# Performance work log

Measured on AMD Instinct MI355X. Metric: run time of the kernel, lower is better.

## Reference

```python
import jax, jax.numpy as jnp
import numpy as np

EMBED_DIM = 768
NUM_HEADS = 12
PROJ_DIM = EMBED_DIM // NUM_HEADS  # 64
M_FEATURES = 128
EPS = 1e-6


def _orthogonal_projection(key, m, d):
    # Faithful to create_projection_matrix(scaling=0): stacked transposed Q-factors
    # of iid gaussian blocks, rescaled by chi-distributed row norms.
    nb_full_blocks = m // d
    keys = jax.random.split(key, nb_full_blocks + 2)
    blocks = []
    for i in range(nb_full_blocks):
        q, _ = jnp.linalg.qr(jax.random.normal(keys[i], (d, d)))
        blocks.append(q.T)
    rem = m - nb_full_blocks * d
    if rem > 0:
        q, _ = jnp.linalg.qr(jax.random.normal(keys[nb_full_blocks], (d, d)))
        blocks.append(q.T[:rem])
    final = jnp.vstack(blocks)
    multiplier = jnp.linalg.norm(jax.random.normal(keys[-1], (m, d)), axis=1)
    return multiplier[:, None] * final


def setup_inputs() -> dict:
    key = jax.random.key(0)
    ks = jax.random.split(key, 8)
    B, L, E = 4, 4096, EMBED_DIM
    s = 1.0 / np.sqrt(E)
    inp = {
        "x": jax.random.normal(ks[0], (B, L, E), jnp.float32),
        "Wq": jax.random.normal(ks[1], (E, E), jnp.float32) * s,
        "bq": jnp.zeros((E,), jnp.float32),
        "Wk": jax.random.normal(ks[2], (E, E), jnp.float32) * s,
        "bk": jnp.zeros((E,), jnp.float32),
        "Wv": jax.random.normal(ks[3], (E, E), jnp.float32) * s,
        "bv": jnp.zeros((E,), jnp.float32),
        "Wo": jax.random.normal(ks[4], (E, E), jnp.float32) * s,
        "bo": jnp.zeros((E,), jnp.float32),
        "proj": _orthogonal_projection(ks[5], M_FEATURES, PROJ_DIM),
    }
    return inp


def _softmax_kernel(data, projection_matrix):
    # data: [B, L, H, D]; projection_matrix: [M, D]
    data_normalizer = 1.0 / jnp.sqrt(jnp.sqrt(jnp.float32(PROJ_DIM)))
    data = data_normalizer * data
    ratio = 1.0 / jnp.sqrt(jnp.float32(projection_matrix.shape[0]))
    data_dash = jnp.einsum("blhd,md->blhm", data, projection_matrix)
    diag_data = jnp.sum(jnp.square(data), axis=-1, keepdims=True) / 2.0  # [B,L,H,1]
    stab = jnp.max(data_dash, axis=-1, keepdims=True)
    return ratio * (jnp.exp(data_dash - diag_data - stab) + EPS)


def reference(x, Wq, bq, Wk, bk, Wv, bv, Wo, bo, proj):
    B, L, E = x.shape
    H, D = NUM_HEADS, PROJ_DIM

    def split_heads(t):
        return t.reshape(B, L, H, D)

    q = split_heads(x @ Wq + bq)
    k = split_heads(x @ Wk + bk)
    v = split_heads(x @ Wv + bv)

    q_prime = _softmax_kernel(q, proj)  # [B,L,H,M]
    k_prime = _softmax_kernel(k, proj)  # [B,L,H,M]

    # Linear-attention numerator/denominator (O(L) in sequence length).
    kvs = jnp.einsum("blhm,blhd->bhmd", k_prime, v)          # [B,H,M,D]
    num = jnp.einsum("blhm,bhmd->blhd", q_prime, kvs)        # [B,L,H,D]
    ks_sum = jnp.sum(k_prime, axis=1)                         # [B,H,M]
    den = jnp.einsum("blhm,bhm->blh", q_prime, ks_sum)        # [B,L,H]
    attention = num / den[..., None]                          # [B,L,H,D]

    # Faithful to source: transpose to [B,H,L,D] then reshape to [B,-1,E].
    concat = jnp.transpose(attention, (0, 2, 1, 3)).reshape(B, -1, E)
    return concat @ Wo + bo
```

## Files before the change

kernel.cpp:

```cpp
#include <hip/hip_runtime.h>

typedef _Float16 f16;
typedef __attribute__((ext_vector_type(8))) _Float16 half8;
typedef __attribute__((ext_vector_type(4))) _Float16 half4;
typedef __attribute__((ext_vector_type(4))) float f32x4;

#define DEVINL static __device__ __forceinline__

constexpr float NORMALIZER = 0.35355339059327373f;
constexpr float RATIO      = 0.08838834764831845f;
constexpr float FEPS       = 1e-6f;

constexpr size_t OFF_WQKVT = 0;
constexpr size_t OFF_WOT   = OFF_WQKVT + (size_t)2304*768*2;
constexpr size_t OFF_PROJF = OFF_WOT   + (size_t)768*768*2;
constexpr size_t OFF_KS    = OFF_PROJF + (size_t)128*64*2;
constexpr size_t OFF_KSP   = OFF_KS    + (size_t)48*128*4;
constexpr size_t OFF_KVST  = OFF_KSP   + (size_t)48*64*128*4;
constexpr size_t OFF_KVSP  = OFF_KVST  + (size_t)48*64*128*2;
constexpr size_t OFF_X16   = OFF_KVSP  + (size_t)16*48*128*64*4;
constexpr size_t OFF_ATT   = OFF_X16;
constexpr size_t OFF_Q16   = OFF_X16 + (size_t)16384*768*2;
constexpr size_t OFF_K16   = OFF_Q16 + (size_t)16384*768*2;
constexpr size_t OFF_VT    = OFF_K16 + (size_t)16384*768*2;
constexpr size_t OFF_KPT   = OFF_VT  + (size_t)16384*768*2;

DEVINL void gload_lds16(const f16* g, f16* lds) {
  __builtin_amdgcn_global_load_lds(
      (const __attribute__((address_space(1))) void*)g,
      (__attribute__((address_space(3))) void*)lds, 16, 0, 0);
}

#define VMCNT0    asm volatile("s_waitcnt vmcnt(0)" ::: "memory")
#define BAR       __builtin_amdgcn_s_barrier()

DEVINL void gemm128_core(const f16* __restrict__ Ag, const f16* __restrict__ Bg,
                         f16* smem, f32x4 (&acc)[4][3], int w, int lane)
{
  constexpr int NT = 24;
  const int wm = w >> 2, wn = w & 3;
  const int c = lane & 15, g16 = lane >> 4;
  const int tid = threadIdx.x;

#pragma unroll
  for (int i = 0; i < 4; ++i)
#pragma unroll
    for (int j = 0; j < 3; ++j)
      acc[i][j] = f32x4{0.f, 0.f, 0.f, 0.f};

  auto SA = [&](int tt, f16* buf) {
    const int r = tid >> 2, sg = tid & 3;
    const int seg = sg ^ ((r >> 1) & 3);
    gload_lds16(Ag + (size_t)r * 768 + tt * 32 + seg * 8, buf + w * 64 * 8);
  };
  auto SB = [&](int tt, f16* buf) {
    {
      const int r = tid >> 2, sg = tid & 3;
      const int seg = sg ^ ((r >> 1) & 3);
      gload_lds16(Bg + (size_t)r * 768 + tt * 32 + seg * 8, buf + 4096 + w * 64 * 8);
    }
    if (w < 4) {
      const int id = 512 + tid;
      const int r = id >> 2, sg = id & 3;
      const int seg = sg ^ ((r >> 1) & 3);
      gload_lds16(Bg + (size_t)r * 768 + tt * 32 + seg * 8, buf + 4096 + (512 + w * 64) * 8);
    }
  };
  auto RDA = [&](const f16* buf, int mh, half8 (&av)[4]) {
#pragma unroll
    for (int i = 0; i < 4; ++i) {
      const int r = wm * 64 + mh * 32 + i * 16 + c;
      av[i] = *(const half8*)(buf + r * 32 + ((g16 ^ ((r >> 1) & 3)) << 3));
    }
  };
  auto RDB = [&](const f16* buf, half8 (&bv)[3]) {
#pragma unroll
    for (int j = 0; j < 3; ++j) {
      const int r = wn * 48 + j * 16 + c;
      bv[j] = *(const half8*)(buf + 4096 + r * 32 + ((g16 ^ ((r >> 1) & 3)) << 3));
    }
  };

  SA(0, smem); SB(0, smem);
  VMCNT0;
  BAR;

#pragma unroll 1
  for (int t = 0; t < NT; ++t) {
    f16* bufR = smem + (t & 1) * 10240;
    f16* bufW = smem + ((t & 1) ^ 1) * 10240;
    const bool st = (t + 1) < NT;
    half8 av[4], bv[3];

    RDA(bufR, 0, av); RDB(bufR, bv);
    if (st) SA(t + 1, bufW);
    __builtin_amdgcn_s_setprio(1);
#pragma unroll
    for (int i = 0; i < 2; ++i)
#pragma unroll
      for (int j = 0; j < 3; ++j)
        acc[i][j] = __builtin_amdgcn_mfma_f32_16x16x32_f16(av[i], bv[j], acc[i][j], 0, 0, 0);
    __builtin_amdgcn_s_setprio(0);
    if (st) SB(t + 1, bufW);
    __builtin_amdgcn_s_setprio(1);
#pragma unroll
    for (int i = 2; i < 4; ++i)
#pragma unroll
      for (int j = 0; j < 3; ++j)
        acc[i][j] = __builtin_amdgcn_mfma_f32_16x16x32_f16(av[i], bv[j], acc[i][j], 0, 0, 0);
    __builtin_amdgcn_s_setprio(0);
    VMCNT0;
    BAR;
  }
}

__global__ __launch_bounds__(512, 4) void k_gemm_qkv6(const f16* __restrict__ X16, const f16* __restrict__ WT,
    const float* __restrict__ bq, const float* __restrict__ bk, const float* __restrict__ bv,
    f16* __restrict__ Qo, f16* __restrict__ Ko, f16* __restrict__ VT)
{
  __shared__ f16 smem[20480];
  f32x4 acc[4][3];
  const int lin = blockIdx.x;
  const int xcd = lin & 7, chunk = lin >> 3;
  const int bx = xcd * 16 + chunk / 12;
  const int by = chunk % 12;
  const int brow0 = bx * 128;
  const int tid = threadIdx.x, w = tid >> 6, lane = tid & 63;
  gemm128_core(X16 + (size_t)brow0 * 768, WT + (size_t)by * 192 * 768, smem, acc, w, lane);

  const int wm = w >> 2, wn = w & 3;
  const int c = lane & 15, g16 = lane >> 4;
  const int which = by >> 2;
  const int colhdr = (by & 3) * 192;
  const float* bias = which == 0 ? bq : (which == 1 ? bk : bv);
  float bb[3];
#pragma unroll
  for (int j = 0; j < 3; ++j) bb[j] = bias[colhdr + wn * 48 + j * 16 + c];

  f16* ep = smem;
  if (which < 2) {
    f16* QK = which == 0 ? Qo : Ko;
#pragma unroll 1
    for (int p = 0; p < 2; ++p) {
      __syncthreads();
      if (wm == p) {
#pragma unroll
        for (int i = 0; i < 4; ++i)
#pragma unroll
          for (int j = 0; j < 3; ++j)
#pragma unroll
            for (int r = 0; r < 4; ++r)
              ep[(i * 16 + g16 * 4 + r) * 200 + wn * 48 + j * 16 + c] = (f16)(acc[i][j][r] + bb[j]);
      }
      __syncthreads();
      const int row = tid >> 3, c8 = (tid & 7) * 24;
      f16* dst = QK + (size_t)(brow0 + p * 64 + row) * 768 + colhdr + c8;
      const f16* sp = ep + row * 200 + c8;
#pragma unroll
      for (int u = 0; u < 3; ++u) *(half8*)(dst + u * 8) = *(const half8*)(sp + u * 8);
    }
  } else {
    const int bIdx = brow0 >> 12;
#pragma unroll 1
    for (int ch = 0; ch < 2; ++ch) {
      __syncthreads();
      if ((wn >> 1) == ch) {
#pragma unroll
        for (int i = 0; i < 4; ++i)
#pragma unroll
          for (int j = 0; j < 3; ++j)
#pragma unroll
            for (int r = 0; r < 4; ++r)
              ep[((wn & 1) * 48 + j * 16 + c) * 136 + wm * 64 + i * 16 + g16 * 4 + r]
                  = (f16)(acc[i][j][r] + bb[j]);
      }
      __syncthreads();
      if (tid < 384) {
        const int cl = tid >> 2, sg = (tid & 3) * 32;
        const int vcol = colhdr + ch * 96 + cl;
        const int h = vcol >> 6, d = vcol & 63;
        f16* dst = VT + ((size_t)(bIdx * 12 + h) * 64 + d) * 4096 + (brow0 & 4095) + sg;
        const f16* sp = ep + cl * 136 + sg;
#pragma unroll
        for (int u = 0; u < 4; ++u) *(half8*)(dst + u * 8) = *(const half8*)(sp + u * 8);
      }
    }
  }
}

__global__ __launch_bounds__(512, 4) void k_gemm_out6(const f16* __restrict__ ATT, const f16* __restrict__ WOT,
    const float* __restrict__ bo, float* __restrict__ out)
{
  __shared__ f16 smem[20480];
  f32x4 acc[4][3];
  const int lin = blockIdx.x;
  const int xcd = lin & 7, chunk = lin >> 3;
  const int bx = xcd * 16 + (chunk >> 2);
  const int by = chunk & 3;
  const int brow0 = bx * 128;
  const int tid = threadIdx.x, w = tid >> 6, lane = tid & 63;
  gemm128_core(ATT + (size_t)brow0 * 768, WOT + (size_t)by * 192 * 768, smem, acc, w, lane);

  const int wm = w >> 2, wn = w & 3;
  const int c = lane & 15, g16 = lane >> 4;
  float bb[3];
#pragma unroll
  for (int j = 0; j < 3; ++j) bb[j] = bo[by * 192 + wn * 48 + j * 16 + c];
#pragma unroll
  for (int i = 0; i < 4; ++i) {
    const int row0 = brow0 + wm * 64 + i * 16 + g16 * 4;
#pragma unroll
    for (int j = 0; j < 3; ++j) {
      const int col = by * 192 + wn * 48 + j * 16 + c;
#pragma unroll
      for (int r = 0; r < 4; ++r)
        out[(size_t)(row0 + r) * 768 + col] = acc[i][j][r] + bb[j];
    }
  }
}

template<int BN>
DEVINL void gemm_tile(const f16* A, int lda, const f16* Bt, int ldb, int K,
                      f16* As, f16* Bs, f32x4 (&acc)[4][BN/32])
{
  constexpr int NF = BN/32;
  const int t = threadIdx.x;
  const int w = t >> 6, lane = t & 63;
  const int g = lane >> 4, c = lane & 15;
  const int wr = w >> 1, wc = w & 1;
  const int srow = lane >> 2;
  const int sseg = (lane & 3) * 8;

#pragma unroll
  for (int i = 0; i < 4; ++i)
#pragma unroll
    for (int j = 0; j < NF; ++j)
      acc[i][j] = f32x4{0.f, 0.f, 0.f, 0.f};

  for (int k0 = 0; k0 < K; k0 += 32) {
#pragma unroll
    for (int r = 0; r < 2; ++r) {
      const int rowblk = (w + 4*r) * 16;
      gload_lds16(A + (size_t)(rowblk + srow) * lda + k0 + sseg, As + rowblk*32);
    }
#pragma unroll
    for (int r = 0; r < BN/64; ++r) {
      const int rowblk = (w + 4*r) * 16;
      gload_lds16(Bt + (size_t)(rowblk + srow) * ldb + k0 + sseg, Bs + rowblk*32);
    }
    __syncthreads();
    half8 av[4], bv[NF];
#pragma unroll
    for (int i = 0; i < 4; ++i)
      av[i] = *(const half8*)(As + (wr*64 + i*16 + c)*32 + g*8);
#pragma unroll
    for (int j = 0; j < NF; ++j)
      bv[j] = *(const half8*)(Bs + (wc*(BN/2) + j*16 + c)*32 + g*8);
#pragma unroll
    for (int i = 0; i < 4; ++i)
#pragma unroll
      for (int j = 0; j < NF; ++j)
        acc[i][j] = __builtin_amdgcn_mfma_f32_16x16x32_f16(av[i], bv[j], acc[i][j], 0, 0, 0);
    __syncthreads();
  }
}

__global__ __launch_bounds__(256) void k_cast_x(const float* __restrict__ X, f16* __restrict__ X16)
{
  const size_t i = ((size_t)blockIdx.x*256 + threadIdx.x) * 4;
  const float4 v = *(const float4*)(X + i);
  half4 h;
  h[0] = (f16)v.x; h[1] = (f16)v.y; h[2] = (f16)v.z; h[3] = (f16)v.w;
  *(half4*)(X16 + i) = h;
}

__global__ __launch_bounds__(256) void k_transpose_w4(const float* __restrict__ Wq, const float* __restrict__ Wk,
    const float* __restrict__ Wv, const float* __restrict__ Wo, f16* __restrict__ WQKVT, f16* __restrict__ WOT)
{
  __shared__ float ls[64][65];
  const int t = threadIdx.x;
  const int k0 = blockIdx.x*64, n0 = blockIdx.y*64, z = blockIdx.z;
  const float* W = z == 0 ? Wq : (z == 1 ? Wk : (z == 2 ? Wv : Wo));
  f16* Wt = z < 3 ? (WQKVT + (size_t)z*768*768) : WOT;
#pragma unroll
  for (int it = 0; it < 4; ++it) {
    const int r = it*16 + (t >> 4);
    const int cs = (t & 15) * 4;
    const float4 v = *(const float4*)(W + (size_t)(k0 + r)*768 + n0 + cs);
    ls[r][cs+0] = v.x; ls[r][cs+1] = v.y; ls[r][cs+2] = v.z; ls[r][cs+3] = v.w;
  }
  __syncthreads();
  const int n = t >> 2;
  const int seg = (t & 3) * 16;
  half8 ov[2];
#pragma unroll
  for (int i = 0; i < 16; ++i) ov[i>>3][i&7] = (f16)ls[seg + i][n];
  f16* dst = Wt + (size_t)(n0 + n)*768 + k0 + seg;
  *(half8*)dst = ov[0];
  *(half8*)(dst + 8) = ov[1];
}

__global__ __launch_bounds__(256) void k_cast_proj(const float* __restrict__ P, f16* __restrict__ PF)
{
  const int i = blockIdx.x*256 + threadIdx.x;
  PF[i] = (f16)(NORMALIZER * P[i]);
}

DEVINL void feat_common(const f16* base, const f16* PROJF,
                        f16* qs, f16* ps, float* dd, float* diag_s)
{
  const int t = threadIdx.x, w = t >> 6, lane = t & 63;
#pragma unroll
  for (int it = 0; it < 2; ++it) {
    const int rowblk = it*32 + w*8;
    gload_lds16(base + (size_t)(rowblk + (lane>>3))*768 + (lane&7)*8, qs + rowblk*64);
  }
#pragma unroll
  for (int it = 0; it < 4; ++it) {
    const int rowblk = it*32 + w*8;
    gload_lds16(PROJF + (size_t)(rowblk + (lane>>3))*64 + (lane&7)*8, ps + rowblk*64);
  }
  __syncthreads();
  if (t < 64) {
    float s = 0.f;
    for (int d = 0; d < 64; ++d) { const float qv = (float)qs[t*64 + d]; s += qv*qv; }
    diag_s[t] = 0.0625f * s;
  }
  const int g = lane >> 4, c = lane & 15;
  const int wr = w >> 1, wc = w & 1;
  f32x4 facc[2][4];
#pragma unroll
  for (int i = 0; i < 2; ++i)
#pragma unroll
    for (int j = 0; j < 4; ++j) facc[i][j] = f32x4{0.f,0.f,0.f,0.f};
#pragma unroll
  for (int kk = 0; kk < 2; ++kk) {
    half8 av[2], bv[4];
#pragma unroll
    for (int i = 0; i < 2; ++i) av[i] = *(const half8*)(qs + (wr*32 + i*16 + c)*64 + kk*32 + g*8);
#pragma unroll
    for (int j = 0; j < 4; ++j) bv[j] = *(const half8*)(ps + (wc*64 + j*16 + c)*64 + kk*32 + g*8);
#pragma unroll
    for (int i = 0; i < 2; ++i)
#pragma unroll
      for (int j = 0; j < 4; ++j)
        facc[i][j] = __builtin_amdgcn_mfma_f32_16x16x32_f16(av[i], bv[j], facc[i][j], 0, 0, 0);
  }
#pragma unroll
  for (int i = 0; i < 2; ++i)
#pragma unroll
    for (int j = 0; j < 4; ++j)
#pragma unroll
      for (int r = 0; r < 4; ++r)
        dd[(wr*32 + i*16 + g*4 + r)*129 + wc*64 + j*16 + c] = facc[i][j][r];
  __syncthreads();
}

__global__ __launch_bounds__(256) void k_kfeat(const f16* __restrict__ Kin, const f16* __restrict__ PROJF,
    f16* __restrict__ KPT, float* __restrict__ KSP)
{
  __shared__ f16 qs[64*64];
  __shared__ f16 ps[128*64];
  __shared__ float dd[64*129];
  __shared__ float diag_s[64];
  const int t = threadIdx.x;
  const int lb = blockIdx.x, bh = blockIdx.y;
  const int b = bh / 12, h = bh - b*12;
  feat_common(Kin + ((size_t)(b*4096 + lb*64))*768 + h*64, PROJF, qs, ps, dd, diag_s);
  const int l = t >> 2, s = t & 3;
  float v[32];
#pragma unroll
  for (int j = 0; j < 32; ++j) v[j] = dd[l*129 + s*32 + j];
  float mx = v[0];
#pragma unroll
  for (int j = 1; j < 32; ++j) mx = fmaxf(mx, v[j]);
  mx = fmaxf(mx, __shfl_xor(mx, 1));
  mx = fmaxf(mx, __shfl_xor(mx, 2));
  const float off = diag_s[l] + mx;
#pragma unroll
  for (int j = 0; j < 32; ++j) dd[l*129 + s*32 + j] = RATIO * (__expf(v[j] - off) + FEPS);
  __syncthreads();
  if (t < 128) {
    float sm = 0.f;
    for (int l2 = 0; l2 < 64; ++l2) sm += dd[l2*129 + t];
    KSP[((size_t)bh*64 + lb)*128 + t] = sm;
  }
  const int m = t >> 1, hf = t & 1;
  half8 ov[4];
#pragma unroll
  for (int i2 = 0; i2 < 32; ++i2) ov[i2>>3][i2&7] = (f16)dd[(hf*32 + i2)*129 + m];
  f16* dst = KPT + ((size_t)bh*128 + m)*4096 + lb*64 + hf*32;
#pragma unroll
  for (int q8 = 0; q8 < 4; ++q8) *(half8*)(dst + q8*8) = ov[q8];
}

__global__ __launch_bounds__(256) void k_kvs(const f16* __restrict__ KPT, const f16* __restrict__ VT,
    float* __restrict__ KVSP)
{
  __shared__ f16 As[128*32], Bs[64*32];
  f32x4 acc[4][2];
  const int chunk = blockIdx.x, bh = blockIdx.y;
  gemm_tile<64>(KPT + (size_t)bh*128*4096 + chunk*256, 4096,
                VT  + (size_t)bh*64*4096  + chunk*256, 4096, 256, As, Bs, acc);
  const int t = threadIdx.x, w = t>>6, lane = t&63, g = lane>>4, c = lane&15;
  const int wr = w>>1, wc = w&1;
  float* dst = KVSP + (size_t)(chunk*48 + bh)*128*64;
#pragma unroll
  for (int i = 0; i < 4; ++i) {
    const int row0 = wr*64 + i*16 + g*4;
#pragma unroll
    for (int j = 0; j < 2; ++j) {
      const int col = wc*32 + j*16 + c;
#pragma unroll
      for (int r = 0; r < 4; ++r) dst[(size_t)(row0 + r)*64 + col] = acc[i][j][r];
    }
  }
}

__global__ __launch_bounds__(256) void k_reduce(const float* __restrict__ KVSP, const float* __restrict__ KSP,
    f16* __restrict__ KVST, float* __restrict__ KS)
{
  const int i = blockIdx.x*256 + threadIdx.x;
  if (i < 48*128*64) {
    const int bh = i >> 13, md = i & 8191, m = md >> 6, d = md & 63;
    float s = 0.f;
#pragma unroll
    for (int c = 0; c < 16; ++c) s += KVSP[((size_t)(c*48 + bh)*128 + m)*64 + d];
    KVST[((size_t)bh*64 + d)*128 + m] = (f16)s;
  }
  if (i < 48*128) {
    const int bh = i >> 7, m = i & 127;
    float s = 0.f;
#pragma unroll 8
    for (int lb = 0; lb < 64; ++lb) s += KSP[((size_t)bh*64 + lb)*128 + m];
    KS[i] = s;
  }
}

__global__ __launch_bounds__(256) void k_qfn(const f16* __restrict__ Q, const f16* __restrict__ PROJF,
    const float* __restrict__ KS, const f16* __restrict__ KVST, f16* __restrict__ ATT)
{
  __shared__ f16 qs[64*64];
  __shared__ f16 ps[128*64];
  __shared__ float dd[64*129];
  __shared__ float diag_s[64];
  __shared__ float den_s[64];
  __shared__ f16 qp[64*128];
  __shared__ float ks_s[128];
  const int t = threadIdx.x;
  const int lb = blockIdx.x, bh = blockIdx.y;
  const int b = bh / 12, h = bh - b*12;
  if (t < 128) ks_s[t] = KS[bh*128 + t];
  feat_common(Q + ((size_t)(b*4096 + lb*64))*768 + h*64, PROJF, qs, ps, dd, diag_s);

  const int w = t >> 6, lane = t & 63, g16 = lane >> 4, c = lane & 15;
  const int wr = w >> 1, wc = w & 1;
  half8 bv2[2][4];
#pragma unroll
  for (int j = 0; j < 2; ++j) {
    const int d = wc*32 + j*16 + c;
#pragma unroll
    for (int kk = 0; kk < 4; ++kk)
      bv2[j][kk] = *(const half8*)(KVST + (size_t)bh*8192 + d*128 + kk*32 + g16*8);
  }

  const int l = t >> 2, s = t & 3;
  float v[32];
#pragma unroll
  for (int j = 0; j < 32; ++j) v[j] = dd[l*129 + s*32 + j];
  float mx = v[0];
#pragma unroll
  for (int j = 1; j < 32; ++j) mx = fmaxf(mx, v[j]);
  mx = fmaxf(mx, __shfl_xor(mx, 1));
  mx = fmaxf(mx, __shfl_xor(mx, 2));
  const float off = diag_s[l] + mx;
  half8 ov[4];
  float dp = 0.f;
#pragma unroll
  for (int j = 0; j < 32; ++j) {
    const float e = RATIO * (__expf(v[j] - off) + FEPS);
    ov[j>>3][j&7] = (f16)e;
    dp += e * ks_s[s*32 + j];
  }
  dp += __shfl_xor(dp, 1);
  dp += __shfl_xor(dp, 2);
  if (s == 0) den_s[l] = dp;
#pragma unroll
  for (int k = 0; k < 4; ++k)
    *(half8*)(qp + l*128 + (((4*s + k) ^ (l & 7)) << 3)) = ov[k];
  __syncthreads();

  f32x4 acc2[2][2];
#pragma unroll
  for (int i = 0; i < 2; ++i)
#pragma unroll
    for (int j = 0; j < 2; ++j) acc2[i][j] = f32x4{0.f,0.f,0.f,0.f};
#pragma unroll
  for (int kk = 0; kk < 4; ++kk) {
    half8 av2[2];
#pragma unroll
    for (int i = 0; i < 2; ++i) {
      const int l2 = wr*32 + i*16 + c;
      av2[i] = *(const half8*)(qp + l2*128 + (((kk*4 + g16) ^ (l2 & 7)) << 3));
    }
#pragma unroll
    for (int i = 0; i < 2; ++i)
#pragma unroll
      for (int j = 0; j < 2; ++j)
        acc2[i][j] = __builtin_amdgcn_mfma_f32_16x16x32_f16(av2[i], bv2[j][kk], acc2[i][j], 0, 0, 0);
  }

  f16* ep = ps;
#pragma unroll
  for (int i = 0; i < 2; ++i)
#pragma unroll
    for (int j = 0; j < 2; ++j)
#pragma unroll
      for (int r = 0; r < 4; ++r) {
        const int l3 = wr*32 + i*16 + g16*4 + r;
        ep[l3*72 + wc*32 + j*16 + c] = (f16)(acc2[i][j][r] / den_s[l3]);
      }
  __syncthreads();
  const int row = t >> 2, sg = (t & 3) * 16;
  f16* dst = ATT + ((size_t)bh*4096 + lb*64 + row)*64 + sg;
  const f16* sp = ep + row*72 + sg;
  *(half8*)dst = *(const half8*)sp;
  *(half8*)(dst + 8) = *(const half8*)(sp + 8);
}

extern "C" void kernel_launch(void* const* d_in, const int* in_sizes, int n_in,
                              void* d_out, int out_size, void* d_ws, size_t ws_size,
                              hipStream_t stream)
{
  const float* x    = (const float*)d_in[0];
  const float* Wq   = (const float*)d_in[1];
  const float* bq   = (const float*)d_in[2];
  const float* Wk   = (const float*)d_in[3];
  const float* bk   = (const float*)d_in[4];
  const float* Wv   = (const float*)d_in[5];
  const float* bv   = (const float*)d_in[6];
  const float* Wo   = (const float*)d_in[7];
  const float* bo   = (const float*)d_in[8];
  const float* proj = (const float*)d_in[9];
  float* out = (float*)d_out;
  char* ws = (char*)d_ws;

  f16*   WQKVT = (f16*)(ws + OFF_WQKVT);
  f16*   WOT   = (f16*)(ws + OFF_WOT);
  f16*   PROJF = (f16*)(ws + OFF_PROJF);
  float* KS    = (float*)(ws + OFF_KS);
  float* KSP   = (float*)(ws + OFF_KSP);
  f16*   KVST  = (f16*)(ws + OFF_KVST);
  float* KVSP  = (float*)(ws + OFF_KVSP);
  f16*   X16   = (f16*)(ws + OFF_X16);
  f16*   ATT   = (f16*)(ws + OFF_ATT);
  f16*   Q16   = (f16*)(ws + OFF_Q16);
  f16*   K16   = (f16*)(ws + OFF_K16);
  f16*   VT    = (f16*)(ws + OFF_VT);
  f16*   KPT   = (f16*)(ws + OFF_KPT);

  k_cast_x<<<12288, 256, 0, stream>>>(x, X16);
  k_transpose_w4<<<dim3(12,12,4), 256, 0, stream>>>(Wq, Wk, Wv, Wo, WQKVT, WOT);
  k_cast_proj<<<32, 256, 0, stream>>>(proj, PROJF);

  k_gemm_qkv6<<<1536, 512, 0, stream>>>(X16, WQKVT, bq, bk, bv, Q16, K16, VT);
  k_kfeat<<<dim3(64,48), 256, 0, stream>>>(K16, PROJF, KPT, KSP);
  k_kvs<<<dim3(16,48), 256, 0, stream>>>(KPT, VT, KVSP);
  k_reduce<<<1536, 256, 0, stream>>>(KVSP, KSP, KVST, KS);
  k_qfn<<<dim3(64,48), 256, 0, stream>>>(Q16, PROJF, KS, KVST, ATT);
  k_gemm_out6<<<512, 512, 0, stream>>>(ATT, WOT, bo, out);
}
```

Baseline: 255.5 us.

## Enlarge GEMM block tile to 256 rows for QKV and output projections

The shared GEMM core now computes a 256x192 tile per 512-thread block instead of 128x192. Each wave holds 8x3 accumulators and reads A fragments in two halves per k-step. This halves the grid size and reuses each B tile across twice as many rows, cutting redundant weight loads and LDS traffic per output. In exchange it raises register and LDS use, may hurt occupancy, and the out-projection now launches only 256 blocks, which may underfill the GPU.

Measured after the change: 440.8 us. 72.5% more time.

```diff
diff --git a/kernel.cpp b/kernel.cpp
--- a/kernel.cpp
+++ b/kernel.cpp
@@ -34,8 +34,8 @@
 #define VMCNT0    asm volatile("s_waitcnt vmcnt(0)" ::: "memory")
 #define BAR       __builtin_amdgcn_s_barrier()
 
-DEVINL void gemm128_core(const f16* __restrict__ Ag, const f16* __restrict__ Bg,
-                         f16* smem, f32x4 (&acc)[4][3], int w, int lane)
+DEVINL void gemm256c(const f16* __restrict__ Ag, const f16* __restrict__ Bg,
+                     f16* smem, f32x4 (&acc)[8][3], int w, int lane)
 {
   constexpr int NT = 24;
   const int wm = w >> 2, wn = w & 3;
@@ -43,33 +43,37 @@
   const int tid = threadIdx.x;
 
 #pragma unroll
-  for (int i = 0; i < 4; ++i)
+  for (int i = 0; i < 8; ++i)
 #pragma unroll
     for (int j = 0; j < 3; ++j)
       acc[i][j] = f32x4{0.f, 0.f, 0.f, 0.f};
 
   auto SA = [&](int tt, f16* buf) {
-    const int r = tid >> 2, sg = tid & 3;
-    const int seg = sg ^ ((r >> 1) & 3);
-    gload_lds16(Ag + (size_t)r * 768 + tt * 32 + seg * 8, buf + w * 64 * 8);
+#pragma unroll
+    for (int u = 0; u < 2; ++u) {
+      const int id = u * 512 + tid;
+      const int r = id >> 2, sg = id & 3;
+      const int seg = sg ^ ((r >> 1) & 3);
+      gload_lds16(Ag + (size_t)r * 768 + tt * 32 + seg * 8, buf + (u * 512 + w * 64) * 8);
+    }
   };
   auto SB = [&](int tt, f16* buf) {
     {
       const int r = tid >> 2, sg = tid & 3;
       const int seg = sg ^ ((r >> 1) & 3);
-      gload_lds16(Bg + (size_t)r * 768 + tt * 32 + seg * 8, buf + 4096 + w * 64 * 8);
+      gload_lds16(Bg + (size_t)r * 768 + tt * 32 + seg * 8, buf + 8192 + w * 64 * 8);
     }
     if (w < 4) {
       const int id = 512 + tid;
       const int r = id >> 2, sg = id & 3;
       const int seg = sg ^ ((r >> 1) & 3);
-      gload_lds16(Bg + (size_t)r * 768 + tt * 32 + seg * 8, buf + 4096 + (512 + w * 64) * 8);
+      gload_lds16(Bg + (size_t)r * 768 + tt * 32 + seg * 8, buf + 8192 + (512 + w * 64) * 8);
     }
   };
   auto RDA = [&](const f16* buf, int mh, half8 (&av)[4]) {
 #pragma unroll
     for (int i = 0; i < 4; ++i) {
-      const int r = wm * 64 + mh * 32 + i * 16 + c;
+      const int r = wm * 128 + mh * 64 + i * 16 + c;
       av[i] = *(const half8*)(buf + r * 32 + ((g16 ^ ((r >> 1) & 3)) << 3));
     }
   };
@@ -77,7 +81,7 @@
 #pragma unroll
     for (int j = 0; j < 3; ++j) {
       const int r = wn * 48 + j * 16 + c;
-      bv[j] = *(const half8*)(buf + 4096 + r * 32 + ((g16 ^ ((r >> 1) & 3)) << 3));
+      bv[j] = *(const half8*)(buf + 8192 + r * 32 + ((g16 ^ ((r >> 1) & 3)) << 3));
     }
   };
 
@@ -87,8 +91,8 @@
 
 #pragma unroll 1
   for (int t = 0; t < NT; ++t) {
-    f16* bufR = smem + (t & 1) * 10240;
-    f16* bufW = smem + ((t & 1) ^ 1) * 10240;
+    f16* bufR = smem + (t & 1) * 14336;
+    f16* bufW = smem + ((t & 1) ^ 1) * 14336;
     const bool st = (t + 1) < NT;
     half8 av[4], bv[3];
 
@@ -96,37 +100,38 @@
     if (st) SA(t + 1, bufW);
     __builtin_amdgcn_s_setprio(1);
 #pragma unroll
-    for (int i = 0; i < 2; ++i)
+    for (int i = 0; i < 4; ++i)
 #pragma unroll
       for (int j = 0; j < 3; ++j)
         acc[i][j] = __builtin_amdgcn_mfma_f32_16x16x32_f16(av[i], bv[j], acc[i][j], 0, 0, 0);
     __builtin_amdgcn_s_setprio(0);
+    RDA(bufR, 1, av);
     if (st) SB(t + 1, bufW);
     __builtin_amdgcn_s_setprio(1);
 #pragma unroll
-    for (int i = 2; i < 4; ++i)
+    for (int i = 0; i < 4; ++i)
 #pragma unroll
       for (int j = 0; j < 3; ++j)
-        acc[i][j] = __builtin_amdgcn_mfma_f32_16x16x32_f16(av[i], bv[j], acc[i][j], 0, 0, 0);
+        acc[4 + i][j] = __builtin_amdgcn_mfma_f32_16x16x32_f16(av[i], bv[j], acc[4 + i][j], 0, 0, 0);
     __builtin_amdgcn_s_setprio(0);
     VMCNT0;
     BAR;
   }
 }
 
-__global__ __launch_bounds__(512, 4) void k_gemm_qkv6(const f16* __restrict__ X16, const f16* __restrict__ WT,
+__global__ __launch_bounds__(512, 4) void k_gemm_qkv7(const f16* __restrict__ X16, const f16* __restrict__ WT,
     const float* __restrict__ bq, const float* __restrict__ bk, const float* __restrict__ bv,
     f16* __restrict__ Qo, f16* __restrict__ Ko, f16* __restrict__ VT)
 {
-  __shared__ f16 smem[20480];
-  f32x4 acc[4][3];
+  __shared__ f16 smem[28672];
+  f32x4 acc[8][3];
   const int lin = blockIdx.x;
   const int xcd = lin & 7, chunk = lin >> 3;
-  const int bx = xcd * 16 + chunk / 12;
+  const int bx = xcd * 8 + chunk / 12;
   const int by = chunk % 12;
-  const int brow0 = bx * 128;
-  const int tid = threadIdx.x, w = tid >> 6, lane = tid & 63;
-  gemm128_core(X16 + (size_t)brow0 * 768, WT + (size_t)by * 192 * 768, smem, acc, w, lane);
+  const int brow0 = bx * 256;
+  const int t = threadIdx.x, w = t >> 6, lane = t & 63;
+  gemm256c(X16 + (size_t)brow0 * 768, WT + (size_t)by * 192 * 768, smem, acc, w, lane);
 
   const int wm = w >> 2, wn = w & 3;
   const int c = lane & 15, g16 = lane >> 4;
@@ -145,61 +150,62 @@
       __syncthreads();
       if (wm == p) {
 #pragma unroll
-        for (int i = 0; i < 4; ++i)
+        for (int ii = 0; ii < 8; ++ii)
 #pragma unroll
           for (int j = 0; j < 3; ++j)
 #pragma unroll
             for (int r = 0; r < 4; ++r)
-              ep[(i * 16 + g16 * 4 + r) * 200 + wn * 48 + j * 16 + c] = (f16)(acc[i][j][r] + bb[j]);
+              ep[((ii >> 2) * 64 + (ii & 3) * 16 + g16 * 4 + r) * 200 + wn * 48 + j * 16 + c]
+                  = (f16)(acc[ii][j][r] + bb[j]);
       }
       __syncthreads();
-      const int row = tid >> 3, c8 = (tid & 7) * 24;
-      f16* dst = QK + (size_t)(brow0 + p * 64 + row) * 768 + colhdr + c8;
-      const f16* sp = ep + row * 200 + c8;
-#pragma unroll
-      for (int u = 0; u < 3; ++u) *(half8*)(dst + u * 8) = *(const half8*)(sp + u * 8);
+      const int row = t >> 2, sg = (t & 3) * 48;
+      f16* dst = QK + (size_t)(brow0 + p * 128 + row) * 768 + colhdr + sg;
+      const f16* sp = ep + row * 200 + sg;
+#pragma unroll
+      for (int u = 0; u < 6; ++u) *(half8*)(dst + u * 8) = *(const half8*)(sp + u * 8);
     }
   } else {
     const int bIdx = brow0 >> 12;
 #pragma unroll 1
-    for (int ch = 0; ch < 2; ++ch) {
+    for (int p = 0; p < 2; ++p) {
       __syncthreads();
-      if ((wn >> 1) == ch) {
-#pragma unroll
-        for (int i = 0; i < 4; ++i)
+      if (wm == p) {
+#pragma unroll
+        for (int ii = 0; ii < 8; ++ii)
 #pragma unroll
           for (int j = 0; j < 3; ++j)
 #pragma unroll
             for (int r = 0; r < 4; ++r)
-              ep[((wn & 1) * 48 + j * 16 + c) * 136 + wm * 64 + i * 16 + g16 * 4 + r]
-                  = (f16)(acc[i][j][r] + bb[j]);
+              ep[(wn * 48 + j * 16 + c) * 136 + (ii >> 2) * 64 + (ii & 3) * 16 + g16 * 4 + r]
+                  = (f16)(acc[ii][j][r] + bb[j]);
       }
       __syncthreads();
-      if (tid < 384) {
-        const int cl = tid >> 2, sg = (tid & 3) * 32;
-        const int vcol = colhdr + ch * 96 + cl;
+      if (t < 384) {
+        const int cl = t >> 1, sg = (t & 1) * 64;
+        const int vcol = colhdr + cl;
         const int h = vcol >> 6, d = vcol & 63;
-        f16* dst = VT + ((size_t)(bIdx * 12 + h) * 64 + d) * 4096 + (brow0 & 4095) + sg;
+        f16* dst = VT + ((size_t)(bIdx * 12 + h) * 64 + d) * 4096 + (brow0 & 4095) + p * 128 + sg;
         const f16* sp = ep + cl * 136 + sg;
 #pragma unroll
-        for (int u = 0; u < 4; ++u) *(half8*)(dst + u * 8) = *(const half8*)(sp + u * 8);
+        for (int u = 0; u < 8; ++u) *(half8*)(dst + u * 8) = *(const half8*)(sp + u * 8);
       }
     }
   }
 }
 
-__global__ __launch_bounds__(512, 4) void k_gemm_out6(const f16* __restrict__ ATT, const f16* __restrict__ WOT,
+__global__ __launch_bounds__(512, 4) void k_gemm_out7(const f16* __restrict__ ATT, const f16* __restrict__ WOT,
     const float* __restrict__ bo, float* __restrict__ out)
 {
-  __shared__ f16 smem[20480];
-  f32x4 acc[4][3];
+  __shared__ f16 smem[28672];
+  f32x4 acc[8][3];
   const int lin = blockIdx.x;
   const int xcd = lin & 7, chunk = lin >> 3;
-  const int bx = xcd * 16 + (chunk >> 2);
+  const int bx = xcd * 8 + (chunk >> 2);
   const int by = chunk & 3;
-  const int brow0 = bx * 128;
-  const int tid = threadIdx.x, w = tid >> 6, lane = tid & 63;
-  gemm128_core(ATT + (size_t)brow0 * 768, WOT + (size_t)by * 192 * 768, smem, acc, w, lane);
+  const int brow0 = bx * 256;
+  const int t = threadIdx.x, w = t >> 6, lane = t & 63;
+  gemm256c(ATT + (size_t)brow0 * 768, WOT + (size_t)by * 192 * 768, smem, acc, w, lane);
 
   const int wm = w >> 2, wn = w & 3;
   const int c = lane & 15, g16 = lane >> 4;
@@ -207,14 +213,14 @@
 #pragma unroll
   for (int j = 0; j < 3; ++j) bb[j] = bo[by * 192 + wn * 48 + j * 16 + c];
 #pragma unroll
-  for (int i = 0; i < 4; ++i) {
-    const int row0 = brow0 + wm * 64 + i * 16 + g16 * 4;
+  for (int ii = 0; ii < 8; ++ii) {
+    const int row0 = brow0 + wm * 128 + (ii >> 2) * 64 + (ii & 3) * 16 + g16 * 4;
 #pragma unroll
     for (int j = 0; j < 3; ++j) {
       const int col = by * 192 + wn * 48 + j * 16 + c;
 #pragma unroll
       for (int r = 0; r < 4; ++r)
-        out[(size_t)(row0 + r) * 768 + col] = acc[i][j][r] + bb[j];
+        out[(size_t)(row0 + r) * 768 + col] = acc[ii][j][r] + bb[j];
     }
   }
 }
@@ -563,10 +569,10 @@
   k_transpose_w4<<<dim3(12,12,4), 256, 0, stream>>>(Wq, Wk, Wv, Wo, WQKVT, WOT);
   k_cast_proj<<<32, 256, 0, stream>>>(proj, PROJF);
 
-  k_gemm_qkv6<<<1536, 512, 0, stream>>>(X16, WQKVT, bq, bk, bv, Q16, K16, VT);
+  k_gemm_qkv7<<<768, 512, 0, stream>>>(X16, WQKVT, bq, bk, bv, Q16, K16, VT);
   k_kfeat<<<dim3(64,48), 256, 0, stream>>>(K16, PROJF, KPT, KSP);
   k_kvs<<<dim3(16,48), 256, 0, stream>>>(KPT, VT, KVSP);
   k_reduce<<<1536, 256, 0, stream>>>(KVSP, KSP, KVST, KS);
   k_qfn<<<dim3(64,48), 256, 0, stream>>>(Q16, PROJF, KS, KVST, ATT);
-  k_gemm_out6<<<512, 512, 0, stream>>>(ATT, WOT, bo, out);
-}
+  k_gemm_out7<<<256, 512, 0, stream>>>(ATT, WOT, bo, out);
+}
```
